# Kernel optimization log

Hardware: AMD Instinct MI355X
Metric: run time of the kernel (lower is better)

## Reference

```python
import jax, jax.numpy as jnp
import numpy as np

HEADS = 8
HEAD_DIM = 64
WINDOW = 65  # odd


def setup_inputs() -> dict:
    key = jax.random.key(0)
    k1, k2, k3 = jax.random.split(key, 3)
    B, S, D_MODEL = 2, 2048, HEADS * HEAD_DIM
    x = jax.random.normal(k1, (B, S, D_MODEL), dtype=jnp.float32)
    W_qkv = jax.random.normal(k2, (D_MODEL, 3 * HEADS * HEAD_DIM), dtype=jnp.float32) * (1.0 / np.sqrt(D_MODEL))
    W_out = jax.random.normal(k3, (HEADS * HEAD_DIM, D_MODEL), dtype=jnp.float32) * (1.0 / np.sqrt(HEADS * HEAD_DIM))
    b_out = jnp.zeros((D_MODEL,), dtype=jnp.float32)
    return {"x": x, "W_qkv": W_qkv, "W_out": W_out, "b_out": b_out}


def reference(x, W_qkv, W_out, b_out):
    B, S, _ = x.shape
    H, D, W = HEADS, HEAD_DIM, WINDOW
    pad = W // 2

    qkv = x @ W_qkv                              # [B,S,3*H*D]
    qkv = qkv.reshape(B, S, H, 3 * D)
    q, k, v = jnp.split(qkv, 3, axis=-1)          # each [B,S,H,D]

    # zero-pad along sequence (matches tf.pad; padded keys get score 0, NOT -inf)
    k_pad = jnp.pad(k, ((0, 0), (pad, pad), (0, 0), (0, 0)))
    v_pad = jnp.pad(v, ((0, 0), (pad, pad), (0, 0), (0, 0)))

    # sliding windows via gather: [S, W] indices into padded seq (= tf.signal.frame)
    idx = jnp.arange(S)[:, None] + jnp.arange(W)[None, :]
    k_win = k_pad[:, idx]                         # [B,S,W,H,D]
    v_win = v_pad[:, idx]                         # [B,S,W,H,D]

    scale = 1.0 / jnp.sqrt(jnp.asarray(D, dtype=x.dtype))
    scores = jnp.einsum('bshd,bswhd->bhsw', q, k_win) * scale  # [B,H,S,W]
    weights = jax.nn.softmax(scores, axis=-1)
    attn = jnp.einsum('bhsw,bswhd->bshd', weights, v_win)       # [B,S,H,D]
    attn = attn.reshape(B, S, H * D)
    return attn @ W_out + b_out
```

## Files before the change

kernel.cpp:

```cpp
#include <hip/hip_runtime.h>
#include <hip/hip_bf16.h>
#include <stdint.h>

typedef short short8 __attribute__((ext_vector_type(8)));
typedef float f32x4 __attribute__((ext_vector_type(4)));
typedef unsigned short ushort4_t __attribute__((ext_vector_type(4)));
typedef unsigned short ushort8_t __attribute__((ext_vector_type(8)));

#define S_LEN 2048
#define NQKV 1536
#define DMODEL 512

__device__ inline unsigned short f2bf(float f) {
  unsigned int u = __float_as_uint(f);
  unsigned int r = (u + 0x7FFFu + ((u >> 16) & 1u)) >> 16;
  return (unsigned short)r;
}

__device__ __forceinline__ void gll16(const unsigned short* g, unsigned short* l) {
  __builtin_amdgcn_global_load_lds(
      (const __attribute__((address_space(1))) unsigned int*)g,
      (__attribute__((address_space(3))) unsigned int*)l, 16, 0, 0);
}

__global__ __launch_bounds__(256) void k_prep(const float* __restrict__ x,
                                              unsigned short* __restrict__ xb,
                                              const float* __restrict__ w1,
                                              unsigned short* __restrict__ o1,
                                              const float* __restrict__ w2,
                                              unsigned short* __restrict__ o2,
                                              unsigned short* __restrict__ Kp,
                                              unsigned short* __restrict__ Vp) {
  __shared__ float T[32][33];
  int bid = blockIdx.x;
  int t = threadIdx.x;
  if (bid < 1024) {
    int i = (bid * 256 + t) * 8;
    float4 a = *(const float4*)(x + i);
    float4 b = *(const float4*)(x + i + 4);
    ushort8_t o;
    o[0] = f2bf(a.x); o[1] = f2bf(a.y); o[2] = f2bf(a.z); o[3] = f2bf(a.w);
    o[4] = f2bf(b.x); o[5] = f2bf(b.y); o[6] = f2bf(b.z); o[7] = f2bf(b.w);
    *(ushort8_t*)(xb + i) = o;
    return;
  }
  if (bid >= 2048) {
    int p = bid - 2048;
    ushort8_t z = {};
    if (p < 16) {
      unsigned short* dst = Kp + (size_t)p * 2112 * 64;
#pragma unroll
      for (int i = 0; i < 2; i++) {
        int s = t + 256 * i;
        int row = s >> 3, c = s & 7;
        int r2 = row < 32 ? row : row - 32 + 2080;
        *(ushort8_t*)&dst[r2 * 64 + c * 8] = z;
      }
    } else {
      unsigned short* dst = Vp + (size_t)(p - 16) * 64 * 2112;
#pragma unroll
      for (int i = 0; i < 2; i++) {
        int s = t + 256 * i;
        int d = s >> 3, side = (s >> 2) & 1, c = s & 3;
        *(ushort8_t*)&dst[(size_t)d * 2112 + side * 2080 + c * 8] = z;
      }
    }
    return;
  }
  bid -= 1024;
  int bx = bid & 63, byy = bid >> 6;
  const float* w; unsigned short* o; int cols;
  if (bx < 48) { w = w1; o = o1; cols = 1536; }
  else         { w = w2; o = o2; cols = 512; bx -= 48; }
  int r0 = byy * 32, c0 = bx * 32;
  int tr = t / 32, tc = t % 32;
#pragma unroll
  for (int i = 0; i < 4; i++) {
    int r = tr + i * 8;
    T[r][tc] = w[(size_t)(r0 + r) * cols + c0 + tc];
  }
  __syncthreads();
#pragma unroll
  for (int i = 0; i < 4; i++) {
    int rr = tr + i * 8;
    o[(size_t)(c0 + rr) * 512 + r0 + tc] = f2bf(T[tc][rr]);
  }
}

template <int BM, int MODE>
__global__ __launch_bounds__(256) void k_gemm(const unsigned short* __restrict__ A,
                                              const unsigned short* __restrict__ Bt,
                                              void* __restrict__ Cout,
                                              const float* __restrict__ bias,
                                              unsigned short* __restrict__ qs,
                                              unsigned short* __restrict__ kp,
                                              unsigned short* __restrict__ vp,
                                              int M, int N, int K) {
  constexpr int MR = BM / 32;
  constexpr int CA = BM / 64;
  constexpr int STAGE_SH = 2 * BM * 32 + 2 * 128 * 32;
  constexpr int BOUNCE_SH = 16384;
  constexpr int SMEM_SH = STAGE_SH > BOUNCE_SH ? STAGE_SH : BOUNCE_SH;
  __shared__ __align__(16) unsigned short smem[SMEM_SH];
  const int ASZ = BM * 32, BOFF = 2 * BM * 32, BSZ = 128 * 32;

  const int t = threadIdx.x, lane = t & 63, wid = t >> 6;
  const int m0 = blockIdx.y * BM, n0 = blockIdx.x * 128;
  const int wm = (wid >> 1) * (BM / 2), wn = (wid & 1) * 64;
  const int lr = lane & 15, kr = (lane >> 4) * 8, lg = lane >> 4;
  const unsigned short* Ab = A + (size_t)m0 * K;
  const unsigned short* Bb = Bt + (size_t)n0 * K;
  f32x4 acc[MR][4] = {};

  const int NT = K / 32;
  auto stage = [&](int buf, int kt) {
#pragma unroll
    for (int c = 0; c < CA; c++) {
      int f = t + 256 * c;
      gll16(Ab + (size_t)(f >> 2) * K + kt + (f & 3) * 8, &smem[buf * ASZ + f * 8]);
    }
#pragma unroll
    for (int c = 0; c < 2; c++) {
      int f = t + 256 * c;
      gll16(Bb + (size_t)(f >> 2) * K + kt + (f & 3) * 8, &smem[BOFF + buf * BSZ + f * 8]);
    }
  };

  stage(0, 0);
  int buf = 0;
  for (int it = 0; it < NT; ++it) {
    __syncthreads();
    if (it + 1 < NT) stage(buf ^ 1, (it + 1) * 32);
    const unsigned short* Ap = &smem[buf * ASZ];
    const unsigned short* Bp = &smem[BOFF + buf * BSZ];
    short8 af[MR], bfv[4];
#pragma unroll
    for (int i = 0; i < MR; i++)
      af[i] = *(const short8*)&Ap[(wm + i * 16 + lr) * 32 + kr];
#pragma unroll
    for (int i = 0; i < 4; i++)
      bfv[i] = *(const short8*)&Bp[(wn + i * 16 + lr) * 32 + kr];
#pragma unroll
    for (int mi = 0; mi < MR; mi++)
#pragma unroll
      for (int ni = 0; ni < 4; ni++)
        acc[mi][ni] = __builtin_amdgcn_mfma_f32_16x16x32_bf16(af[mi], bfv[ni], acc[mi][ni], 0, 0, 0);
    buf ^= 1;
  }

  if (MODE == 0) {
    __syncthreads();
    float* ft = (float*)smem;
#pragma unroll
    for (int mi = 0; mi < MR; mi++)
#pragma unroll
      for (int ni = 0; ni < 4; ni++)
#pragma unroll
        for (int j = 0; j < 4; j++)
          ft[(wm + mi * 16 + lg * 4 + j) * 128 + wn + ni * 16 + lr] = acc[mi][ni][j];
    __syncthreads();
#pragma unroll
    for (int i = 0; i < BM / 8; i++) {
      int s = t + 256 * i;
      int row = s >> 5, ch = s & 31;
      float4 v = *(const float4*)&ft[row * 128 + ch * 4];
      float4 bv = *(const float4*)&bias[n0 + ch * 4];
      v.x += bv.x; v.y += bv.y; v.z += bv.z; v.w += bv.w;
      *(float4*)&((float*)Cout)[(size_t)(m0 + row) * N + n0 + ch * 4] = v;
    }
  } else {
    __syncthreads();
#pragma unroll
    for (int mi = 0; mi < MR; mi++)
#pragma unroll
      for (int ni = 0; ni < 4; ni++)
#pragma unroll
        for (int j = 0; j < 4; j++) {
          int row = wm + mi * 16 + lg * 4 + j;
          int col = wn + ni * 16 + lr;
          smem[row * 128 + (col ^ (((row >> 3) & 7) << 3))] = f2bf(acc[mi][ni][j]);
        }
    __syncthreads();

    const int b_ = m0 >> 11;
    const int posb = m0 & 2047;
#pragma unroll
    for (int hf = 0; hf < 2; hf++) {
      int c_abs = n0 + hf * 64;
      int h = c_abs / 192, seg = (c_abs % 192) >> 6;
      if (seg < 2) {
        unsigned short* dst = (seg == 0)
            ? qs + ((size_t)(b_ * 8 + h) * 2048 + posb) * 64
            : kp + ((size_t)(b_ * 8 + h) * 2112 + 32 + posb) * 64;
#pragma unroll
        for (int i = 0; i < 4; i++) {
          int s = t + 256 * i;
          int row = s >> 3, ch = s & 7;
          int src = row * 128 + ((hf * 64 + ch * 8) ^ (((row >> 3) & 7) << 3));
          *(ushort8_t*)&dst[s * 8] = *(const ushort8_t*)&smem[src];
        }
      } else {
        unsigned short* dst = vp + (size_t)(b_ * 8 + h) * 64 * 2112;
#pragma unroll
        for (int i = 0; i < 4; i++) {
          int s = t + 256 * i;
          int dl = s >> 4, pc = s & 15;
          ushort8_t v;
#pragma unroll
          for (int j = 0; j < 8; j++) {
            int row = pc * 8 + j;
            v[j] = smem[row * 128 + ((hf * 64 + dl) ^ (((row >> 3) & 7) << 3))];
          }
          *(ushort8_t*)&dst[(size_t)dl * 2112 + 32 + posb + pc * 8] = v;
        }
      }
    }
  }
}

__global__ __launch_bounds__(256) void k_attn(const unsigned short* __restrict__ Qs,
                                              const unsigned short* __restrict__ Kp,
                                              const unsigned short* __restrict__ Vp,
                                              unsigned short* __restrict__ attnb) {
  __shared__ __align__(16) unsigned short Kt[128 * 64];
  __shared__ __align__(16) unsigned short Vt[64 * 192];
  __shared__ __align__(16) unsigned short Qt[64 * 64];
  const int t = threadIdx.x, lane = t & 63, w = t >> 6;
  const int blk = blockIdx.x;
  const int sbi = blk & 31, h = (blk >> 5) & 7, b = blk >> 8;
  const int sb = sbi * 64;
  const int bh = b * 8 + h;
  const int lr = lane & 15, lg = lane >> 4;

  {
    const unsigned short* src = Kp + ((size_t)bh * 2112 + sb) * 64;
#pragma unroll
    for (int i = 0; i < 4; i++) {
      int s = t + 256 * i, row = s >> 3, c = s & 7;
      gll16(src + row * 64 + (c ^ (row & 7)) * 8, &Kt[s * 8]);
    }
  }
  {
    const unsigned short* src = Vp + (size_t)bh * 64 * 2112 + sb;
#pragma unroll
    for (int i = 0; i < 6; i++) {
      int s = t + 256 * i, d = s / 24, c = s - d * 24;
      gll16(src + (size_t)d * 2112 + (c ^ (d & 7)) * 8, &Vt[s * 8]);
    }
  }
  {
    const unsigned short* src = Qs + ((size_t)bh * 2048 + sb) * 64;
#pragma unroll
    for (int i = 0; i < 2; i++) {
      int s = t + 256 * i, row = s >> 3, c = s & 7;
      gll16(src + row * 64 + (c ^ (row & 7)) * 8, &Qt[s * 8]);
    }
  }
  __syncthreads();

  const int sw = (lr & 7) << 3;

  short8 qb[2];
#pragma unroll
  for (int ks = 0; ks < 2; ks++)
    qb[ks] = *(const short8*)&Qt[(w * 16 + lr) * 64 + ((ks * 32 + lg * 8) ^ sw)];

  f32x4 sc[5] = {};
#pragma unroll
  for (int ct = 0; ct < 5; ct++) {
#pragma unroll
    for (int ks = 0; ks < 2; ks++) {
      short8 ka = *(const short8*)&Kt[(w * 16 + ct * 16 + lr) * 64 + ((ks * 32 + lg * 8) ^ sw)];
      sc[ct] = __builtin_amdgcn_mfma_f32_16x16x32_bf16(ka, qb[ks], sc[ct], 0, 0, 0);
    }
  }

  float mx = -1e30f;
#pragma unroll
  for (int ct = 0; ct < 5; ct++)
#pragma unroll
    for (int j = 0; j < 4; j++) {
      int c2 = ct * 16 + lg * 4 + j;
      sc[ct][j] = (c2 >= lr && c2 <= lr + 64) ? sc[ct][j] * 0.125f : -1e30f;
      mx = fmaxf(mx, sc[ct][j]);
    }
  mx = fmaxf(mx, __shfl_xor(mx, 16, 64));
  mx = fmaxf(mx, __shfl_xor(mx, 32, 64));

  float pn[5][4];
  float sum = 0.0f;
#pragma unroll
  for (int ct = 0; ct < 5; ct++)
#pragma unroll
    for (int j = 0; j < 4; j++) {
      pn[ct][j] = __expf(sc[ct][j] - mx);
      sum += pn[ct][j];
    }
  sum += __shfl_xor(sum, 16, 64);
  sum += __shfl_xor(sum, 32, 64);
  float inv = 1.0f / sum;

  unsigned int w01[5], w23[5];
#pragma unroll
  for (int ct = 0; ct < 5; ct++) {
    w01[ct] = (unsigned int)f2bf(pn[ct][0] * inv) | ((unsigned int)f2bf(pn[ct][1] * inv) << 16);
    w23[ct] = (unsigned int)f2bf(pn[ct][2] * inv) | ((unsigned int)f2bf(pn[ct][3] * inv) << 16);
  }

  f32x4 oa[4] = {};
  const int h2 = lg & 1, tl = lg >> 1;
  const int sA = 32 * h2 + lr, sB = sA + 16;
#pragma unroll
  for (int ks = 0; ks < 3; ks++) {
    const int T0 = 2 * ks;
    const int T1 = (2 * ks + 1 < 5) ? (2 * ks + 1) : 4;
    unsigned int a0 = __shfl((int)w01[T0], sA, 64), a1 = __shfl((int)w23[T0], sA, 64);
    unsigned int a2 = __shfl((int)w01[T0], sB, 64), a3 = __shfl((int)w23[T0], sB, 64);
    unsigned int b0 = __shfl((int)w01[T1], sA, 64), b1 = __shfl((int)w23[T1], sA, 64);
    unsigned int b2 = __shfl((int)w01[T1], sB, 64), b3 = __shfl((int)w23[T1], sB, 64);
    union { unsigned int u[4]; short8 v; } pb;
    pb.u[0] = tl ? b0 : a0;
    pb.u[1] = tl ? b1 : a1;
    pb.u[2] = tl ? b2 : a2;
    pb.u[3] = tl ? b3 : a3;
    if (ks == 2 && tl) { pb.u[0] = 0; pb.u[1] = 0; pb.u[2] = 0; pb.u[3] = 0; }
    int pofl = w * 16 + ks * 32 + lg * 8;
#pragma unroll
    for (int nt = 0; nt < 4; nt++) {
      short8 va = *(const short8*)&Vt[(nt * 16 + lr) * 192 + (pofl ^ sw)];
      oa[nt] = __builtin_amdgcn_mfma_f32_16x16x32_bf16(va, pb.v, oa[nt], 0, 0, 0);
    }
  }

  const int s0 = sb + w * 16;
#pragma unroll
  for (int nt = 0; nt < 4; nt++) {
    ushort4_t o;
#pragma unroll
    for (int j = 0; j < 4; j++) o[j] = f2bf(oa[nt][j]);
    *(ushort4_t*)&attnb[((size_t)b * S_LEN + s0 + lr) * DMODEL + h * 64 + nt * 16 + lg * 4] = o;
  }
}

extern "C" void kernel_launch(void* const* d_in, const int* in_sizes, int n_in,
                              void* d_out, int out_size, void* d_ws, size_t ws_size,
                              hipStream_t stream) {
  const float* x    = (const float*)d_in[0];
  const float* Wqkv = (const float*)d_in[1];
  const float* Wout = (const float*)d_in[2];
  const float* bout = (const float*)d_in[3];
  char* ws = (char*)d_ws;
  unsigned short* xb    = (unsigned short*)(ws + 0);
  unsigned short* wqkvt = (unsigned short*)(ws + 4194304);
  unsigned short* woutt = (unsigned short*)(ws + 5767168);
  unsigned short* Qs    = (unsigned short*)(ws + 6291456);
  unsigned short* Kp    = (unsigned short*)(ws + 10485760);
  unsigned short* Vp    = (unsigned short*)(ws + 14811136);
  unsigned short* attnb = (unsigned short*)(ws + 19922944);

  hipLaunchKernelGGL(k_prep, dim3(2080), dim3(256), 0, stream,
                     x, xb, Wqkv, wqkvt, Wout, woutt, Kp, Vp);
  hipLaunchKernelGGL((k_gemm<128, 1>), dim3(12, 32), dim3(256), 0, stream,
                     xb, wqkvt, nullptr, (const float*)nullptr, Qs, Kp, Vp, 4096, 1536, 512);
  hipLaunchKernelGGL(k_attn, dim3(512), dim3(256), 0, stream, Qs, Kp, Vp, attnb);
  hipLaunchKernelGGL((k_gemm<64, 0>), dim3(4, 64), dim3(256), 0, stream,
                     attnb, woutt, d_out, bout,
                     (unsigned short*)nullptr, (unsigned short*)nullptr,
                     (unsigned short*)nullptr, 4096, 512, 512);
}
```

Before: 42.34 us.

## Parameterize GEMM N tile and use 64-wide tiles for both projections

Adds a BN template parameter to the GEMM kernel and launches both the QKV and output projections with 64-column tiles, doubling the grid size. Each QKV block now maps to exactly one head segment (q, k or v), simplifying the scatter epilogue with a 64-wide swizzled bounce buffer. The aim is better CU occupancy and fewer tail effects, at the cost of less A-tile reuse per block and more redundant A loads.

```diff
diff --git a/kernel.cpp b/kernel.cpp
--- a/kernel.cpp
+++ b/kernel.cpp
@@ -87,7 +87,7 @@
   }
 }
 
-template <int BM, int MODE>
+template <int BM, int BN, int MODE>
 __global__ __launch_bounds__(256) void k_gemm(const unsigned short* __restrict__ A,
                                               const unsigned short* __restrict__ Bt,
                                               void* __restrict__ Cout,
@@ -96,21 +96,21 @@
                                               unsigned short* __restrict__ kp,
                                               unsigned short* __restrict__ vp,
                                               int M, int N, int K) {
-  constexpr int MR = BM / 32;
-  constexpr int CA = BM / 64;
-  constexpr int STAGE_SH = 2 * BM * 32 + 2 * 128 * 32;
-  constexpr int BOUNCE_SH = 16384;
+  constexpr int MR = BM / 32, NR = BN / 32;
+  constexpr int CA = BM / 64, CB = BN / 64;
+  constexpr int STAGE_SH = 2 * (BM + BN) * 32;
+  constexpr int BOUNCE_SH = MODE == 0 ? BM * BN * 2 : BM * BN;
   constexpr int SMEM_SH = STAGE_SH > BOUNCE_SH ? STAGE_SH : BOUNCE_SH;
   __shared__ __align__(16) unsigned short smem[SMEM_SH];
-  const int ASZ = BM * 32, BOFF = 2 * BM * 32, BSZ = 128 * 32;
+  const int ASZ = BM * 32, BOFF = 2 * BM * 32, BSZ = BN * 32;
 
   const int t = threadIdx.x, lane = t & 63, wid = t >> 6;
-  const int m0 = blockIdx.y * BM, n0 = blockIdx.x * 128;
-  const int wm = (wid >> 1) * (BM / 2), wn = (wid & 1) * 64;
+  const int m0 = blockIdx.y * BM, n0 = blockIdx.x * BN;
+  const int wm = (wid >> 1) * (BM / 2), wn = (wid & 1) * (BN / 2);
   const int lr = lane & 15, kr = (lane >> 4) * 8, lg = lane >> 4;
   const unsigned short* Ab = A + (size_t)m0 * K;
   const unsigned short* Bb = Bt + (size_t)n0 * K;
-  f32x4 acc[MR][4] = {};
+  f32x4 acc[MR][NR] = {};
 
   const int NT = K / 32;
   auto stage = [&](int buf, int kt) {
@@ -120,7 +120,7 @@
       gll16(Ab + (size_t)(f >> 2) * K + kt + (f & 3) * 8, &smem[buf * ASZ + f * 8]);
     }
 #pragma unroll
-    for (int c = 0; c < 2; c++) {
+    for (int c = 0; c < CB; c++) {
       int f = t + 256 * c;
       gll16(Bb + (size_t)(f >> 2) * K + kt + (f & 3) * 8, &smem[BOFF + buf * BSZ + f * 8]);
     }
@@ -133,17 +133,17 @@
     if (it + 1 < NT) stage(buf ^ 1, (it + 1) * 32);
     const unsigned short* Ap = &smem[buf * ASZ];
     const unsigned short* Bp = &smem[BOFF + buf * BSZ];
-    short8 af[MR], bfv[4];
+    short8 af[MR], bfv[NR];
 #pragma unroll
     for (int i = 0; i < MR; i++)
       af[i] = *(const short8*)&Ap[(wm + i * 16 + lr) * 32 + kr];
 #pragma unroll
-    for (int i = 0; i < 4; i++)
+    for (int i = 0; i < NR; i++)
       bfv[i] = *(const short8*)&Bp[(wn + i * 16 + lr) * 32 + kr];
 #pragma unroll
     for (int mi = 0; mi < MR; mi++)
 #pragma unroll
-      for (int ni = 0; ni < 4; ni++)
+      for (int ni = 0; ni < NR; ni++)
         acc[mi][ni] = __builtin_amdgcn_mfma_f32_16x16x32_bf16(af[mi], bfv[ni], acc[mi][ni], 0, 0, 0);
     buf ^= 1;
   }
@@ -154,16 +154,16 @@
 #pragma unroll
     for (int mi = 0; mi < MR; mi++)
 #pragma unroll
-      for (int ni = 0; ni < 4; ni++)
+      for (int ni = 0; ni < NR; ni++)
 #pragma unroll
         for (int j = 0; j < 4; j++)
-          ft[(wm + mi * 16 + lg * 4 + j) * 128 + wn + ni * 16 + lr] = acc[mi][ni][j];
-    __syncthreads();
-#pragma unroll
-    for (int i = 0; i < BM / 8; i++) {
+          ft[(wm + mi * 16 + lg * 4 + j) * BN + wn + ni * 16 + lr] = acc[mi][ni][j];
+    __syncthreads();
+#pragma unroll
+    for (int i = 0; i < BM * BN / 1024; i++) {
       int s = t + 256 * i;
-      int row = s >> 5, ch = s & 31;
-      float4 v = *(const float4*)&ft[row * 128 + ch * 4];
+      int row = s / (BN / 4), ch = s % (BN / 4);
+      float4 v = *(const float4*)&ft[row * BN + ch * 4];
       float4 bv = *(const float4*)&bias[n0 + ch * 4];
       v.x += bv.x; v.y += bv.y; v.z += bv.z; v.w += bv.w;
       *(float4*)&((float*)Cout)[(size_t)(m0 + row) * N + n0 + ch * 4] = v;
@@ -173,46 +173,43 @@
 #pragma unroll
     for (int mi = 0; mi < MR; mi++)
 #pragma unroll
-      for (int ni = 0; ni < 4; ni++)
+      for (int ni = 0; ni < NR; ni++)
 #pragma unroll
         for (int j = 0; j < 4; j++) {
           int row = wm + mi * 16 + lg * 4 + j;
           int col = wn + ni * 16 + lr;
-          smem[row * 128 + (col ^ (((row >> 3) & 7) << 3))] = f2bf(acc[mi][ni][j]);
+          smem[row * 64 + (((col >> 3) ^ ((row >> 3) & 7)) << 3) + (col & 7)] =
+              f2bf(acc[mi][ni][j]);
         }
     __syncthreads();
 
     const int b_ = m0 >> 11;
     const int posb = m0 & 2047;
-#pragma unroll
-    for (int hf = 0; hf < 2; hf++) {
-      int c_abs = n0 + hf * 64;
-      int h = c_abs / 192, seg = (c_abs % 192) >> 6;
-      if (seg < 2) {
-        unsigned short* dst = (seg == 0)
-            ? qs + ((size_t)(b_ * 8 + h) * 2048 + posb) * 64
-            : kp + ((size_t)(b_ * 8 + h) * 2112 + 32 + posb) * 64;
-#pragma unroll
-        for (int i = 0; i < 4; i++) {
-          int s = t + 256 * i;
-          int row = s >> 3, ch = s & 7;
-          int src = row * 128 + ((hf * 64 + ch * 8) ^ (((row >> 3) & 7) << 3));
-          *(ushort8_t*)&dst[s * 8] = *(const ushort8_t*)&smem[src];
+    const int h = n0 / 192, seg = (n0 % 192) >> 6;
+    if (seg < 2) {
+      unsigned short* dst = (seg == 0)
+          ? qs + ((size_t)(b_ * 8 + h) * 2048 + posb) * 64
+          : kp + ((size_t)(b_ * 8 + h) * 2112 + 32 + posb) * 64;
+#pragma unroll
+      for (int i = 0; i < BM / 32; i++) {
+        int s = t + 256 * i;
+        int row = s >> 3, ch = s & 7;
+        int src = row * 64 + ((ch ^ ((row >> 3) & 7)) << 3);
+        *(ushort8_t*)&dst[s * 8] = *(const ushort8_t*)&smem[src];
+      }
+    } else {
+      unsigned short* dst = vp + (size_t)(b_ * 8 + h) * 64 * 2112;
+#pragma unroll
+      for (int i = 0; i < BM / 32; i++) {
+        int s = t + 256 * i;
+        int dl = s / (BM / 8), pc = s % (BM / 8);
+        ushort8_t v;
+#pragma unroll
+        for (int j = 0; j < 8; j++) {
+          int row = pc * 8 + j;
+          v[j] = smem[row * 64 + ((((dl >> 3) ^ (pc & 7)) << 3)) + (dl & 7)];
         }
-      } else {
-        unsigned short* dst = vp + (size_t)(b_ * 8 + h) * 64 * 2112;
-#pragma unroll
-        for (int i = 0; i < 4; i++) {
-          int s = t + 256 * i;
-          int dl = s >> 4, pc = s & 15;
-          ushort8_t v;
-#pragma unroll
-          for (int j = 0; j < 8; j++) {
-            int row = pc * 8 + j;
-            v[j] = smem[row * 128 + ((hf * 64 + dl) ^ (((row >> 3) & 7) << 3))];
-          }
-          *(ushort8_t*)&dst[(size_t)dl * 2112 + 32 + posb + pc * 8] = v;
-        }
+        *(ushort8_t*)&dst[(size_t)dl * 2112 + 32 + posb + pc * 8] = v;
       }
     }
   }
@@ -360,10 +357,10 @@
 
   hipLaunchKernelGGL(k_prep, dim3(2080), dim3(256), 0, stream,
                      x, xb, Wqkv, wqkvt, Wout, woutt, Kp, Vp);
-  hipLaunchKernelGGL((k_gemm<128, 1>), dim3(12, 32), dim3(256), 0, stream,
+  hipLaunchKernelGGL((k_gemm<128, 64, 1>), dim3(24, 32), dim3(256), 0, stream,
                      xb, wqkvt, nullptr, (const float*)nullptr, Qs, Kp, Vp, 4096, 1536, 512);
   hipLaunchKernelGGL(k_attn, dim3(512), dim3(256), 0, stream, Qs, Kp, Vp, attnb);
-  hipLaunchKernelGGL((k_gemm<64, 0>), dim3(4, 64), dim3(256), 0, stream,
+  hipLaunchKernelGGL((k_gemm<64, 64, 0>), dim3(8, 64), dim3(256), 0, stream,
                      attnb, woutt, d_out, bout,
                      (unsigned short*)nullptr, (unsigned short*)nullptr,
                      (unsigned short*)nullptr, 4096, 512, 512);
```

New measurement: 41.92 us. About the same (-1.0%).
